# Optimization experiments

Hardware: AMD Instinct MI355X
Metric: run time of the kernel (lower is better)

## Reference

```python
import jax, jax.numpy as jnp
import numpy as np

N, IN_F, H, D = 3072, 512, 8, 64


def setup_inputs() -> dict:
    key = jax.random.key(0)
    k1, k2, k3, k4, k5 = jax.random.split(key, 5)
    x = jax.random.normal(k1, (N, IN_F), dtype=jnp.float32)
    adj = jax.random.randint(k2, (N, N), 0, 2, dtype=jnp.int32)
    # xavier-uniform-like scales
    s_W = (6.0 / (IN_F + H * D)) ** 0.5
    s_a = (6.0 / (H + D)) ** 0.5
    W = jax.random.uniform(k3, (H * D, IN_F), dtype=jnp.float32, minval=-s_W, maxval=s_W)
    a_src = jax.random.uniform(k4, (H, D), dtype=jnp.float32, minval=-s_a, maxval=s_a)
    a_dst = jax.random.uniform(k5, (H, D), dtype=jnp.float32, minval=-s_a, maxval=s_a)
    return {"x": x, "adj": adj, "W": W, "a_src": a_src, "a_dst": a_dst}


def reference(x, adj, W, a_src, a_dst):
    n = x.shape[0]
    Hh, d = a_src.shape
    h = (x @ W.T).reshape(n, Hh, d)                      # [n, H, d]
    e_src = jnp.einsum('nhd,hd->nh', h, a_src)           # [n, H]
    e_dst = jnp.einsum('nhd,hd->nh', h, a_dst)           # [n, H]
    e = e_src[:, None, :] + e_dst[None, :, :]            # [n, n, H], e[i,j]=src_i+dst_j
    e = jax.nn.leaky_relu(e, negative_slope=0.2)
    mask = (adj + jnp.eye(n, dtype=adj.dtype)) > 0       # [n, n]
    e = jnp.where(mask[:, :, None], e, -jnp.inf)
    alpha = jax.nn.softmax(e, axis=1)                    # softmax over j (neighbors)
    # out[i,h,d] = sum_j alpha[i,j,h] * h[j,h,d]  (dropout=0 / eval mode)
    out = jnp.einsum('ijh,jhd->ihd', alpha, h)
    return out.reshape(n, Hh * d)                        # concat=True
```

## Files before the change

kernel.cpp:

```cpp
#include <hip/hip_runtime.h>
#include <hip/hip_bf16.h>

typedef __bf16 bf16x8 __attribute__((ext_vector_type(8)));
typedef __bf16 bf16x4 __attribute__((ext_vector_type(4)));
typedef _Float16 half8 __attribute__((ext_vector_type(8)));
typedef _Float16 half2v __attribute__((ext_vector_type(2)));
typedef short s16x2 __attribute__((ext_vector_type(2)));
typedef float f32x4 __attribute__((ext_vector_type(4)));
typedef float f32x16 __attribute__((ext_vector_type(16)));

#define NROW 3072
#define NF 512
#define NH 8
#define ND 64
#define GEMM_BLOCKS 384
#define BP_BLOCKS 768

__device__ __forceinline__ unsigned gat_enc_key(float f) {
    unsigned u = __float_as_uint(f);
    return (f < 0.f) ? ~u : (u | 0x80000000u);
}
__device__ __forceinline__ float gat_dec_key(unsigned k) {
    unsigned u = (k & 0x80000000u) ? (k ^ 0x80000000u) : ~k;
    return __uint_as_float(u);
}

__device__ __forceinline__ void gat_ld4(float4 (&d)[4], const float* g, int c) {
#pragma unroll
    for (int t = 0; t < 4; ++t)
        d[t] = *reinterpret_cast<const float4*>(g + t * 8 * NF + c * 32);
}
__device__ __forceinline__ void gat_st4(__bf16* s, const float4 (&v)[4], int wslot) {
#pragma unroll
    for (int t = 0; t < 4; ++t) {
        bf16x4 w = { (__bf16)v[t].x, (__bf16)v[t].y, (__bf16)v[t].z, (__bf16)v[t].w };
        *reinterpret_cast<bf16x4*>(s + t * 320 + wslot) = w;
    }
}
__device__ __forceinline__ void gat_mfma2(const __bf16* sA, const __bf16* sB,
                                          int arow, int half, f32x16& acc) {
#pragma unroll
    for (int ks = 0; ks < 2; ++ks) {
        int q = ((ks << 1) | half) << 3;
        bf16x8 a = *reinterpret_cast<const bf16x8*>(sA + arow + q);
        bf16x8 b = *reinterpret_cast<const bf16x8*>(sB + arow + q);
        acc = __builtin_amdgcn_mfma_f32_32x32x16_bf16(a, b, acc, 0, 0, 0);
    }
}

__global__ __launch_bounds__(256) void gat_gemm_bp(const float* __restrict__ x,
                                                   const float* __restrict__ W,
                                                   _Float16* __restrict__ hT,
                                                   const int* __restrict__ adj,
                                                   unsigned long long* __restrict__ bits64,
                                                   const float* __restrict__ a_src,
                                                   const float* __restrict__ a_dst,
                                                   float* __restrict__ e_srcT,
                                                   float* __restrict__ e_dstT,
                                                   unsigned* __restrict__ maxkey) {
    __shared__ __align__(16) _Float16 smem[10240];
    __shared__ float ered[2][2][2][32];

    int tid = threadIdx.x;
    int wave = tid >> 6;
    int lane = tid & 63;

    if (blockIdx.x >= GEMM_BLOCKS) {
        int row = (blockIdx.x - GEMM_BLOCKS) * 4 + wave;
        const int* p = adj + (long)row * NROW + lane;
        int v[48];
#pragma unroll
        for (int s = 0; s < 48; ++s) v[s] = p[s * 64];
        unsigned long long diag = 1ull << (row & 63);
        int dseg = row >> 6;
#pragma unroll
        for (int s = 0; s < 48; ++s) {
            unsigned long long bal = __ballot(v[s] > 0);
            if (s == dseg) bal |= diag;
            if (lane == 0) bits64[(long)row * 48 + s] = bal;
        }
        return;
    }

    int b = blockIdx.x;
    int i0 = (b >> 3) * 64;
    int o0 = (b & 7) * 64;
    int head = b & 7;
    int half = lane >> 5;
    int l31 = lane & 31;
    int wr = wave >> 1;
    int wc = wave & 1;

    __bf16* sAw = reinterpret_cast<__bf16*>(smem) + wave * 1280;
    __bf16* sBw = reinterpret_cast<__bf16*>(smem) + 5120 + wave * 1280;

    int lr = lane >> 3;
    int lc = (lane & 7) * 4;
    const float* gA = x + (long)(i0 + wr * 32 + lr) * NF + lc;
    const float* gB = W + (long)(o0 + wc * 32 + lr) * NF + lc;
    int wslot = lr * 40 + lc;

    float4 Ae[4], Be[4], Ao[4], Bo[4];
    gat_ld4(Ae, gA, 0); gat_ld4(Be, gB, 0);
    gat_st4(sAw, Ae, wslot); gat_st4(sBw, Be, wslot);
    gat_ld4(Ao, gA, 1); gat_ld4(Bo, gB, 1);
    gat_ld4(Ae, gA, 2); gat_ld4(Be, gB, 2);

    f32x16 acc = {};
    int arow = l31 * 40;

#pragma unroll
    for (int cc = 0; cc < 8; ++cc) {
        int c0 = cc * 2, c1 = c0 + 1;
        gat_mfma2(sAw, sBw, arow, half, acc);
        gat_st4(sAw, Ao, wslot); gat_st4(sBw, Bo, wslot);
        if (c0 + 3 < 16) { gat_ld4(Ao, gA, c0 + 3); gat_ld4(Bo, gB, c0 + 3); }
        gat_mfma2(sAw, sBw, arow, half, acc);
        if (c1 + 1 < 16) {
            gat_st4(sAw, Ae, wslot); gat_st4(sBw, Be, wslot);
            if (c1 + 3 < 16) { gat_ld4(Ae, gA, c1 + 3); gat_ld4(Be, gB, c1 + 3); }
        }
    }

    _Float16* tt = smem + wave * 1280;
#pragma unroll
    for (int reg = 0; reg < 16; ++reg) {
        int rowl = (reg & 3) + 8 * (reg >> 2) + 4 * half;
        tt[rowl * 40 + l31] = (_Float16)acc[reg];
    }
    int orow = lane >> 1;
    int li = (lane & 1) * 16;
    half8 h0, h1;
#pragma unroll
    for (int t = 0; t < 8; ++t) h0[t] = tt[(li + t) * 40 + orow];
#pragma unroll
    for (int t = 0; t < 8; ++t) h1[t] = tt[(li + 8 + t) * 40 + orow];
    _Float16* op = hT + (long)(o0 + wc * 32 + orow) * NROW + i0 + wr * 32 + li;
    *reinterpret_cast<half8*>(op) = h0;
    *reinterpret_cast<half8*>(op + 8) = h1;

    half8 hv0 = *reinterpret_cast<const half8*>(tt + l31 * 40 + half * 16);
    half8 hv1 = *reinterpret_cast<const half8*>(tt + l31 * 40 + half * 16 + 8);
    const float* ap = a_src + head * ND + wc * 32 + half * 16;
    const float* dp = a_dst + head * ND + wc * 32 + half * 16;
    float4 as0 = *reinterpret_cast<const float4*>(ap);
    float4 as1 = *reinterpret_cast<const float4*>(ap + 4);
    float4 as2 = *reinterpret_cast<const float4*>(ap + 8);
    float4 as3 = *reinterpret_cast<const float4*>(ap + 12);
    float4 ad0 = *reinterpret_cast<const float4*>(dp);
    float4 ad1 = *reinterpret_cast<const float4*>(dp + 4);
    float4 ad2 = *reinterpret_cast<const float4*>(dp + 8);
    float4 ad3 = *reinterpret_cast<const float4*>(dp + 12);
    float ps = 0.f, pd = 0.f;
    ps += (float)hv0[0]*as0.x + (float)hv0[1]*as0.y + (float)hv0[2]*as0.z + (float)hv0[3]*as0.w;
    ps += (float)hv0[4]*as1.x + (float)hv0[5]*as1.y + (float)hv0[6]*as1.z + (float)hv0[7]*as1.w;
    ps += (float)hv1[0]*as2.x + (float)hv1[1]*as2.y + (float)hv1[2]*as2.z + (float)hv1[3]*as2.w;
    ps += (float)hv1[4]*as3.x + (float)hv1[5]*as3.y + (float)hv1[6]*as3.z + (float)hv1[7]*as3.w;
    pd += (float)hv0[0]*ad0.x + (float)hv0[1]*ad0.y + (float)hv0[2]*ad0.z + (float)hv0[3]*ad0.w;
    pd += (float)hv0[4]*ad1.x + (float)hv0[5]*ad1.y + (float)hv0[6]*ad1.z + (float)hv0[7]*ad1.w;
    pd += (float)hv1[0]*ad2.x + (float)hv1[1]*ad2.y + (float)hv1[2]*ad2.z + (float)hv1[3]*ad2.w;
    pd += (float)hv1[4]*ad3.x + (float)hv1[5]*ad3.y + (float)hv1[6]*ad3.z + (float)hv1[7]*ad3.w;
    ps += __shfl_xor(ps, 32, 64);
    pd += __shfl_xor(pd, 32, 64);
    if (half == 0) { ered[0][wr][wc][l31] = ps; ered[1][wr][wc][l31] = pd; }
    __syncthreads();
    if (wc == 0) {
        float pst = ered[0][wr][0][l31] + ered[0][wr][1][l31];
        float pdt = ered[1][wr][0][l31] + ered[1][wr][1][l31];
        if (half == 0) {
            e_srcT[head * NROW + i0 + wr * 32 + l31] = pst;
            e_dstT[head * NROW + i0 + wr * 32 + l31] = pdt;
        }
        float mx = pdt;
#pragma unroll
        for (int off = 1; off < 32; off <<= 1) mx = fmaxf(mx, __shfl_xor(mx, off, 64));
        if (lane == 0) atomicMax(&maxkey[head], gat_enc_key(mx));
    }
}

__global__ __launch_bounds__(256) void gat_attn(const unsigned* __restrict__ bits,
                                                const float* __restrict__ e_srcT,
                                                const float* __restrict__ e_dstT,
                                                const unsigned* __restrict__ maxkey,
                                                const _Float16* __restrict__ hT,
                                                _Float16* __restrict__ num,
                                                float* __restrict__ den) {
    constexpr int JCHUNK = NROW / 4;
    constexpr int NC = JCHUNK / 64;
    __shared__ unsigned lds_P[JCHUNK / 2];
    __shared__ unsigned lds_Q[JCHUNK / 2];
    __shared__ __align__(16) _Float16 hbuf[2][4096];
    int b = blockIdx.x;
    int head = b & 7;
    int jc = (b >> 3) & 3;
    int i0 = (b >> 5) * 256;
    int jbase = jc * JCHUNK;
    int tid = threadIdx.x;
    int wave = tid >> 6;
    int lane = tid & 63;
    int half = lane >> 5;
    int l31 = lane & 31;

    float Mg = gat_dec_key(maxkey[head]);
    for (int p = tid; p < JCHUNK / 2; p += 256) {
        float t0 = e_dstT[head * NROW + jbase + 2 * p] - Mg;
        float t1 = e_dstT[head * NROW + jbase + 2 * p + 1] - Mg;
        half2v P = { (_Float16)__expf(t0), (_Float16)__expf(t1) };
        half2v Q = { (_Float16)__expf(0.2f * t0), (_Float16)__expf(0.2f * t1) };
        lds_P[p] = __builtin_bit_cast(unsigned, P);
        lds_Q[p] = __builtin_bit_cast(unsigned, Q);
    }

    int irowA = i0 + wave * 32 + l31;
    int irowB = irowA + 128;
    float uA = e_srcT[head * NROW + irowA] + Mg;
    float uB = e_srcT[head * NROW + irowB] + Mg;
    float RfA = fminf(__expf(-0.8f * uA), 60000.f);
    float RfB = fminf(__expf(-0.8f * uB), 60000.f);
    _Float16 RhA = (_Float16)RfA, RhB = (_Float16)RfB;
    half2v R2A = { RhA, RhA };
    half2v R2B = { RhB, RhB };
    const half8 ones8 = { (_Float16)1.f, (_Float16)1.f, (_Float16)1.f, (_Float16)1.f,
                          (_Float16)1.f, (_Float16)1.f, (_Float16)1.f, (_Float16)1.f };
    const unsigned* browA = bits + (long)irowA * 96 + jc * (JCHUNK / 32);
    const unsigned* browB = bits + (long)irowB * 96 + jc * (JCHUNK / 32);

    int s0 = tid, s1 = tid + 256;
    const _Float16* gp0 = hT + (head * ND + ((s0 >> 6) & 1) * 32 + (s0 & 31)) * NROW
                             + jbase + (s0 >> 7) * 16 + ((s0 >> 5) & 1) * 8;
    const _Float16* gp1 = hT + (head * ND + ((s1 >> 6) & 1) * 32 + (s1 & 31)) * NROW
                             + jbase + (s1 >> 7) * 16 + ((s1 >> 5) & 1) * 8;
    *reinterpret_cast<half8*>(&hbuf[0][tid * 8])         = *reinterpret_cast<const half8*>(gp0);
    *reinterpret_cast<half8*>(&hbuf[0][(tid + 256) * 8]) = *reinterpret_cast<const half8*>(gp1);
    __syncthreads();

    f32x16 acc0a = {}, acc1a = {}, acc2a = {};
    f32x16 acc0b = {}, acc1b = {}, acc2b = {};
    uint2 wmA = *reinterpret_cast<const uint2*>(browA);
    uint2 wmB = *reinterpret_cast<const uint2*>(browB);

    for (int k = 0; k < NC; ++k) {
        half8 st0, st1;
        uint2 wmnA = wmA, wmnB = wmB;
        bool more = (k + 1 < NC);
        if (more) {
            st0 = *reinterpret_cast<const half8*>(gp0 + (k + 1) * 64);
            st1 = *reinterpret_cast<const half8*>(gp1 + (k + 1) * 64);
            wmnA = *reinterpret_cast<const uint2*>(browA + (k + 1) * 2);
            wmnB = *reinterpret_cast<const uint2*>(browB + (k + 1) * 2);
        }
        const _Float16* hb = &hbuf[k & 1][0];
#pragma unroll
        for (int js = 0; js < 4; ++js) {
            int sh = (js & 1) * 16 + half * 8;
            unsigned w8A = (((js < 2) ? wmA.x : wmA.y) >> sh) & 0xffu;
            unsigned w8B = (((js < 2) ? wmB.x : wmB.y) >> sh) & 0xffu;
            unsigned long long S64A = ((unsigned long long)(w8A & 0x55u) << 15)
                                    | ((unsigned long long)(w8A & 0xAAu) << 30);
            unsigned long long S64B = ((unsigned long long)(w8B & 0x55u) << 15)
                                    | ((unsigned long long)(w8B & 0xAAu) << 30);
            uint4 Pv = *reinterpret_cast<const uint4*>(&lds_P[k * 32 + js * 8 + half * 4]);
            uint4 Qv = *reinterpret_cast<const uint4*>(&lds_Q[k * 32 + js * 8 + half * 4]);
            unsigned pr[4] = { Pv.x, Pv.y, Pv.z, Pv.w };
            unsigned qr[4] = { Qv.x, Qv.y, Qv.z, Qv.w };
            unsigned amA[4], amB[4];
#pragma unroll
            for (int t = 0; t < 4; ++t) {
                half2v pv = __builtin_bit_cast(half2v, pr[t]);
                half2v qv = __builtin_bit_cast(half2v, qr[t]);
                half2v mxA = __builtin_elementwise_max(pv, qv * R2A);
                half2v mxB = __builtin_elementwise_max(pv, qv * R2B);
                s16x2 mkA = __builtin_bit_cast(s16x2, (unsigned)(S64A >> (2 * t))) >> 15;
                s16x2 mkB = __builtin_bit_cast(s16x2, (unsigned)(S64B >> (2 * t))) >> 15;
                amA[t] = __builtin_bit_cast(unsigned, mxA) & __builtin_bit_cast(unsigned, mkA);
                amB[t] = __builtin_bit_cast(unsigned, mxB) & __builtin_bit_cast(unsigned, mkB);
            }
            uint4 m4a = { amA[0], amA[1], amA[2], amA[3] };
            uint4 m4b = { amB[0], amB[1], amB[2], amB[3] };
            half8 afA = __builtin_bit_cast(half8, m4a);
            half8 afB = __builtin_bit_cast(half8, m4b);
            half8 v0 = *reinterpret_cast<const half8*>(hb + (js * 128 + lane) * 8);
            half8 v1 = *reinterpret_cast<const half8*>(hb + (js * 128 + 64 + lane) * 8);
            acc0a = __builtin_amdgcn_mfma_f32_32x32x16_f16(afA, v0, acc0a, 0, 0, 0);
            acc1a = __builtin_amdgcn_mfma_f32_32x32x16_f16(afA, v1, acc1a, 0, 0, 0);
            acc2a = __builtin_amdgcn_mfma_f32_32x32x16_f16(afA, ones8, acc2a, 0, 0, 0);
            acc0b = __builtin_amdgcn_mfma_f32_32x32x16_f16(afB, v0, acc0b, 0, 0, 0);
            acc1b = __builtin_amdgcn_mfma_f32_32x32x16_f16(afB, v1, acc1b, 0, 0, 0);
            acc2b = __builtin_amdgcn_mfma_f32_32x32x16_f16(afB, ones8, acc2b, 0, 0, 0);
        }
        if (more) {
            *reinterpret_cast<half8*>(&hbuf[(k + 1) & 1][tid * 8])         = st0;
            *reinterpret_cast<half8*>(&hbuf[(k + 1) & 1][(tid + 256) * 8]) = st1;
        }
        wmA = wmnA;
        wmB = wmnB;
        __syncthreads();
    }

#pragma unroll
    for (int reg = 0; reg < 16; ++reg) {
        int rowl = (reg & 3) + 8 * (reg >> 2) + 4 * half;
        long rbaseA = (long)(jc * NROW + i0 + wave * 32 + rowl);
        long rbaseB = rbaseA + 128;
        if (l31 == 0) {
            den[rbaseA * NH + head] = acc2a[reg];
            den[rbaseB * NH + head] = acc2b[reg];
        }
        long obA = rbaseA * NF + head * ND + l31;
        long obB = rbaseB * NF + head * ND + l31;
        num[obA]      = (_Float16)acc0a[reg];
        num[obA + 32] = (_Float16)acc1a[reg];
        num[obB]      = (_Float16)acc0b[reg];
        num[obB + 32] = (_Float16)acc1b[reg];
    }
}

__global__ __launch_bounds__(256) void gat_final(const _Float16* __restrict__ num,
                                                 const float* __restrict__ den,
                                                 float* __restrict__ out) {
    int idx = (blockIdx.x * 256 + threadIdx.x) * 8;
    int i = idx >> 9;
    int c = idx & 511;
    int head = c >> 6;
    half8 n0 = *reinterpret_cast<const half8*>(num + (long)i * NF + c);
    half8 n1 = *reinterpret_cast<const half8*>(num + (long)(NROW + i) * NF + c);
    half8 n2 = *reinterpret_cast<const half8*>(num + (long)(2 * NROW + i) * NF + c);
    half8 n3 = *reinterpret_cast<const half8*>(num + (long)(3 * NROW + i) * NF + c);
    float ds = den[i * NH + head] + den[(NROW + i) * NH + head]
             + den[(2 * NROW + i) * NH + head] + den[(3 * NROW + i) * NH + head];
    float inv = 1.0f / fmaxf(ds, 1e-30f);
    float r0 = ((float)n0[0] + (float)n1[0] + (float)n2[0] + (float)n3[0]) * inv;
    float r1 = ((float)n0[1] + (float)n1[1] + (float)n2[1] + (float)n3[1]) * inv;
    float r2 = ((float)n0[2] + (float)n1[2] + (float)n2[2] + (float)n3[2]) * inv;
    float r3 = ((float)n0[3] + (float)n1[3] + (float)n2[3] + (float)n3[3]) * inv;
    float r4 = ((float)n0[4] + (float)n1[4] + (float)n2[4] + (float)n3[4]) * inv;
    float r5 = ((float)n0[5] + (float)n1[5] + (float)n2[5] + (float)n3[5]) * inv;
    float r6 = ((float)n0[6] + (float)n1[6] + (float)n2[6] + (float)n3[6]) * inv;
    float r7 = ((float)n0[7] + (float)n1[7] + (float)n2[7] + (float)n3[7]) * inv;
    float4 o0 = { r0, r1, r2, r3 };
    float4 o1 = { r4, r5, r6, r7 };
    *reinterpret_cast<float4*>(out + idx)     = o0;
    *reinterpret_cast<float4*>(out + idx + 4) = o1;
}

extern "C" void kernel_launch(void* const* d_in, const int* in_sizes, int n_in,
                              void* d_out, int out_size, void* d_ws, size_t ws_size,
                              hipStream_t stream) {
    const float* x_raw  = (const float*)d_in[0];
    const int*   adj    = (const int*)d_in[1];
    const float* W_raw  = (const float*)d_in[2];
    const float* as_raw = (const float*)d_in[3];
    const float* ad_raw = (const float*)d_in[4];
    float* out = (float*)d_out;

    char* ws = (char*)d_ws;
    _Float16* hT     = (_Float16*)(ws);
    float*    e_srcT = (float*)(ws + 3145728);
    float*    e_dstT = (float*)(ws + 3244032);
    unsigned* maxkey = (unsigned*)(ws + 3342336);
    unsigned* bits   = (unsigned*)(ws + 3342400);
    _Float16* num    = (_Float16*)(ws + 8192064);
    float*    den    = (float*)(ws + 20774976);

    hipMemsetAsync(maxkey, 0, 64, stream);
    gat_gemm_bp<<<GEMM_BLOCKS + BP_BLOCKS, 256, 0, stream>>>(x_raw, W_raw, hT, adj,
                                                             (unsigned long long*)bits,
                                                             as_raw, ad_raw,
                                                             e_srcT, e_dstT, maxkey);
    gat_attn<<<12 * 4 * 8, 256, 0, stream>>>(bits, e_srcT, e_dstT, maxkey, hT, num, den);
    gat_final<<<NROW * NF / 2048, 256, 0, stream>>>(num, den, out);
}
```

Baseline: 134.2 us.

## Fuse final split-j reduction into attention kernel via last-block atomic counter

```diff
diff --git a/kernel.cpp b/kernel.cpp
--- a/kernel.cpp
+++ b/kernel.cpp
@@ -184,12 +184,15 @@
                                                 const unsigned* __restrict__ maxkey,
                                                 const _Float16* __restrict__ hT,
                                                 _Float16* __restrict__ num,
-                                                float* __restrict__ den) {
+                                                float* __restrict__ den,
+                                                unsigned* __restrict__ counters,
+                                                float* __restrict__ out) {
     constexpr int JCHUNK = NROW / 4;
     constexpr int NC = JCHUNK / 64;
     __shared__ unsigned lds_P[JCHUNK / 2];
     __shared__ unsigned lds_Q[JCHUNK / 2];
     __shared__ __align__(16) _Float16 hbuf[2][4096];
+    __shared__ unsigned done;
     int b = blockIdx.x;
     int head = b & 7;
     int jc = (b >> 3) & 3;
@@ -313,34 +316,42 @@
         num[obB]      = (_Float16)acc0b[reg];
         num[obB + 32] = (_Float16)acc1b[reg];
     }
-}
-
-__global__ __launch_bounds__(256) void gat_final(const _Float16* __restrict__ num,
-                                                 const float* __restrict__ den,
-                                                 float* __restrict__ out) {
-    int idx = (blockIdx.x * 256 + threadIdx.x) * 8;
-    int i = idx >> 9;
-    int c = idx & 511;
-    int head = c >> 6;
-    half8 n0 = *reinterpret_cast<const half8*>(num + (long)i * NF + c);
-    half8 n1 = *reinterpret_cast<const half8*>(num + (long)(NROW + i) * NF + c);
-    half8 n2 = *reinterpret_cast<const half8*>(num + (long)(2 * NROW + i) * NF + c);
-    half8 n3 = *reinterpret_cast<const half8*>(num + (long)(3 * NROW + i) * NF + c);
-    float ds = den[i * NH + head] + den[(NROW + i) * NH + head]
-             + den[(2 * NROW + i) * NH + head] + den[(3 * NROW + i) * NH + head];
-    float inv = 1.0f / fmaxf(ds, 1e-30f);
-    float r0 = ((float)n0[0] + (float)n1[0] + (float)n2[0] + (float)n3[0]) * inv;
-    float r1 = ((float)n0[1] + (float)n1[1] + (float)n2[1] + (float)n3[1]) * inv;
-    float r2 = ((float)n0[2] + (float)n1[2] + (float)n2[2] + (float)n3[2]) * inv;
-    float r3 = ((float)n0[3] + (float)n1[3] + (float)n2[3] + (float)n3[3]) * inv;
-    float r4 = ((float)n0[4] + (float)n1[4] + (float)n2[4] + (float)n3[4]) * inv;
-    float r5 = ((float)n0[5] + (float)n1[5] + (float)n2[5] + (float)n3[5]) * inv;
-    float r6 = ((float)n0[6] + (float)n1[6] + (float)n2[6] + (float)n3[6]) * inv;
-    float r7 = ((float)n0[7] + (float)n1[7] + (float)n2[7] + (float)n3[7]) * inv;
-    float4 o0 = { r0, r1, r2, r3 };
-    float4 o1 = { r4, r5, r6, r7 };
-    *reinterpret_cast<float4*>(out + idx)     = o0;
-    *reinterpret_cast<float4*>(out + idx + 4) = o1;
+
+    __threadfence();
+    __syncthreads();
+    if (tid == 0)
+        done = __hip_atomic_fetch_add(&counters[(b >> 5) * NH + head], 1u,
+                                      __ATOMIC_ACQ_REL, __HIP_MEMORY_SCOPE_AGENT);
+    __syncthreads();
+    if (done == 3u) {
+        __threadfence();
+        for (int e = tid; e < 2048; e += 256) {
+            int row = i0 + (e >> 3);
+            int c0 = (e & 7) * 8;
+            const _Float16* np = num + (long)row * NF + head * ND + c0;
+            half8 n0 = *reinterpret_cast<const half8*>(np);
+            half8 n1 = *reinterpret_cast<const half8*>(np + (long)NROW * NF);
+            half8 n2 = *reinterpret_cast<const half8*>(np + (long)2 * NROW * NF);
+            half8 n3 = *reinterpret_cast<const half8*>(np + (long)3 * NROW * NF);
+            float ds = den[(long)row * NH + head]
+                     + den[(long)(NROW + row) * NH + head]
+                     + den[(long)(2 * NROW + row) * NH + head]
+                     + den[(long)(3 * NROW + row) * NH + head];
+            float inv = 1.0f / fmaxf(ds, 1e-30f);
+            float4 o0, o1;
+            o0.x = ((float)n0[0] + (float)n1[0] + (float)n2[0] + (float)n3[0]) * inv;
+            o0.y = ((float)n0[1] + (float)n1[1] + (float)n2[1] + (float)n3[1]) * inv;
+            o0.z = ((float)n0[2] + (float)n1[2] + (float)n2[2] + (float)n3[2]) * inv;
+            o0.w = ((float)n0[3] + (float)n1[3] + (float)n2[3] + (float)n3[3]) * inv;
+            o1.x = ((float)n0[4] + (float)n1[4] + (float)n2[4] + (float)n3[4]) * inv;
+            o1.y = ((float)n0[5] + (float)n1[5] + (float)n2[5] + (float)n3[5]) * inv;
+            o1.z = ((float)n0[6] + (float)n1[6] + (float)n2[6] + (float)n3[6]) * inv;
+            o1.w = ((float)n0[7] + (float)n1[7] + (float)n2[7] + (float)n3[7]) * inv;
+            float* op = out + (long)row * NF + head * ND + c0;
+            *reinterpret_cast<float4*>(op)     = o0;
+            *reinterpret_cast<float4*>(op + 4) = o1;
+        }
+    }
 }
 
 extern "C" void kernel_launch(void* const* d_in, const int* in_sizes, int n_in,
@@ -358,15 +369,16 @@
     float*    e_srcT = (float*)(ws + 3145728);
     float*    e_dstT = (float*)(ws + 3244032);
     unsigned* maxkey = (unsigned*)(ws + 3342336);
-    unsigned* bits   = (unsigned*)(ws + 3342400);
+    unsigned* counters = maxkey + 16;
+    unsigned* bits   = (unsigned*)(ws + 3342848);
     _Float16* num    = (_Float16*)(ws + 8192064);
     float*    den    = (float*)(ws + 20774976);
 
-    hipMemsetAsync(maxkey, 0, 64, stream);
+    hipMemsetAsync(maxkey, 0, 512, stream);
     gat_gemm_bp<<<GEMM_BLOCKS + BP_BLOCKS, 256, 0, stream>>>(x_raw, W_raw, hT, adj,
                                                              (unsigned long long*)bits,
                                                              as_raw, ad_raw,
                                                              e_srcT, e_dstT, maxkey);
-    gat_attn<<<12 * 4 * 8, 256, 0, stream>>>(bits, e_srcT, e_dstT, maxkey, hT, num, den);
-    gat_final<<<NROW * NF / 2048, 256, 0, stream>>>(num, den, out);
-}
+    gat_attn<<<12 * 4 * 8, 256, 0, stream>>>(bits, e_srcT, e_dstT, maxkey, hT,
+                                             num, den, counters, out);
+}
```

New measurement: 209.6 us. +56.1%, slower.
